# Optimization experiments

Measured on AMD Instinct MI355X. Metric: run time of the kernel, lower is better.

The kernel has to match this reference:

```python
import jax, jax.numpy as jnp
import numpy as np

D_MODEL = 1024
N_HEADS = 16
HEAD_DIM = D_MODEL // N_HEADS


def setup_inputs() -> dict:
    key = jax.random.key(0)
    k_x, k_wqkv, k_bqkv, k_wo, k_bo = jax.random.split(key, 5)
    b, t = 4, 2048
    s = 1.0 / np.sqrt(D_MODEL)
    return {
        "x": jax.random.normal(k_x, (b, t, D_MODEL), dtype=jnp.float32),
        "w_qkv": jax.random.uniform(k_wqkv, (D_MODEL, 3 * D_MODEL), jnp.float32, -s, s),
        "b_qkv": jax.random.uniform(k_bqkv, (3 * D_MODEL,), jnp.float32, -s, s),
        "w_out": jax.random.uniform(k_wo, (D_MODEL, D_MODEL), jnp.float32, -s, s),
        "b_out": jax.random.uniform(k_bo, (D_MODEL,), jnp.float32, -s, s),
    }


def reference(x, w_qkv, b_qkv, w_out, b_out):
    b, t, _ = x.shape
    # fused QKV projection -> [b, t, 3, h, d] -> q,k,v each [b, h, t, d]
    qkv = (x @ w_qkv + b_qkv).reshape(b, t, 3, N_HEADS, HEAD_DIM)
    q, k, v = jnp.moveaxis(qkv, 2, 0)          # each [b, t, h, d]
    q = q.transpose(0, 2, 1, 3)                # [b, h, t, d]
    k = k.transpose(0, 2, 1, 3)
    v = v.transpose(0, 2, 1, 3)
    scale = 1.0 / np.sqrt(HEAD_DIM).astype(np.float32)
    logits = jnp.einsum('bhqd,bhkd->bhqk', q, k) * scale
    causal = jnp.tril(jnp.ones((t, t), dtype=bool))
    logits = jnp.where(causal, logits, jnp.finfo(logits.dtype).min)
    attn = jax.nn.softmax(logits, axis=-1)
    out = jnp.einsum('bhqk,bhkd->bhqd', attn, v)      # [b, h, t, d]
    out = out.transpose(0, 2, 1, 3).reshape(b, t, D_MODEL)
    return out @ w_out + b_out
```

## Files before the change

kernel.cpp:

```cpp
#include <hip/hip_runtime.h>
#include <hip/hip_bf16.h>
#include <math.h>

#define NHEADS 16
#define HDIM   64
#define SEQT   2048
#define NBATCH 4
#define DMODEL 1024
#define MROWS  (NBATCH * SEQT)

typedef __bf16 bf16;
typedef bf16  bf16x8 __attribute__((ext_vector_type(8)));
typedef float f32x4  __attribute__((ext_vector_type(4)));
typedef float f32x16 __attribute__((ext_vector_type(16)));
typedef unsigned int u32x4 __attribute__((ext_vector_type(4)));

#define MFMA_BF16(a, b, c) __builtin_amdgcn_mfma_f32_16x16x32_bf16((a), (b), (c), 0, 0, 0)
#define MFMA32(a, b, c)    __builtin_amdgcn_mfma_f32_32x32x16_bf16((a), (b), (c), 0, 0, 0)
#define Z16 {0.f,0.f,0.f,0.f,0.f,0.f,0.f,0.f,0.f,0.f,0.f,0.f,0.f,0.f,0.f,0.f}
#define LOG2E 1.44269504f

__device__ __forceinline__ void gload_lds16(const void* g, void* l) {
  __builtin_amdgcn_global_load_lds((const __attribute__((address_space(1))) void*)g,
                                   (__attribute__((address_space(3))) void*)l, 16, 0, 0);
}

__device__ __forceinline__ unsigned cvtpk_bf16(float lo, float hi) {
  unsigned r;
  asm("v_cvt_pk_bf16_f32 %0, %1, %2" : "=v"(r) : "v"(lo), "v"(hi));
  return r;
}
__device__ __forceinline__ void plswap(unsigned& a, unsigned& b) {
  asm volatile("v_permlane32_swap_b32 %0, %1" : "+v"(a), "+v"(b));
}
__device__ __forceinline__ float exp2v(float x) {
  float r;
  asm("v_exp_f32 %0, %1" : "=v"(r) : "v"(x));
  return r;
}


__global__ __launch_bounds__(256) void k_cvt_f32_bf16(const float* __restrict__ in,
                                                      bf16* __restrict__ out, int n8) {
  int i = blockIdx.x * blockDim.x + threadIdx.x;
  if (i >= n8) return;
  const float4* in4 = (const float4*)in;
  float4 a = in4[(size_t)i * 2], b = in4[(size_t)i * 2 + 1];
  bf16x8 v;
  v[0] = (bf16)a.x; v[1] = (bf16)a.y; v[2] = (bf16)a.z; v[3] = (bf16)a.w;
  v[4] = (bf16)b.x; v[5] = (bf16)b.y; v[6] = (bf16)b.z; v[7] = (bf16)b.w;
  *(bf16x8*)(out + (size_t)i * 8) = v;
}

__global__ __launch_bounds__(256) void k_transpose_f32_bf16(const float* __restrict__ in,
                                                            bf16* __restrict__ out,
                                                            int R, int C) {
  int nct = C >> 6;
  int rt = blockIdx.x / nct, ct = blockIdx.x % nct;
  __shared__ float tile[64][65];
  int tid = threadIdx.x;
#pragma unroll
  for (int i = 0; i < 16; i++) {
    int e = i * 256 + tid, r = e >> 6, c = e & 63;
    tile[r][c] = in[(size_t)(rt * 64 + r) * C + ct * 64 + c];
  }
  __syncthreads();
#pragma unroll
  for (int i = 0; i < 16; i++) {
    int e = i * 256 + tid, r = e >> 6, c = e & 63;
    out[(size_t)(ct * 64 + r) * R + rt * 64 + c] = (bf16)tile[c][r];
  }
}

__global__ __launch_bounds__(256) void k_transpose_v(const bf16* __restrict__ v,
                                                     bf16* __restrict__ vt) {
  int tt = blockIdx.x & 31;
  int bh = blockIdx.x >> 5;
  __shared__ bf16 tile[64][65];
  int tid = threadIdx.x;
  const bf16* src = v + (size_t)bh * SEQT * 64 + (size_t)tt * 64 * 64;
#pragma unroll
  for (int i = 0; i < 16; i++) {
    int e = i * 256 + tid, r = e >> 6, c = e & 63;
    tile[r][c] = src[r * 64 + c];
  }
  __syncthreads();
  bf16* dst = vt + (size_t)bh * 64 * SEQT + tt * 64;
#pragma unroll
  for (int i = 0; i < 16; i++) {
    int e = i * 256 + tid, r = e >> 6, c = e & 63;
    dst[(size_t)r * SEQT + c] = tile[c][r];
  }
}


__device__ __forceinline__ void gemm128_core(const bf16* __restrict__ A,
                                             const bf16* __restrict__ Bt,
                                             int K, int bm, int bn, char* smem,
                                             f32x4 (&acc)[4][4]) {
  int tid = threadIdx.x, lane = tid & 63, w = tid >> 6;
  int l15 = lane & 15, g = lane >> 4;
  int wrow = (w >> 1) * 64, wcol = (w & 1) * 64;
  char* As = smem;
  char* Bs = smem + 8192;
  const char* Ag = (const char*)(A + (size_t)bm * 128 * K);
  const char* Bg = (const char*)(Bt + (size_t)bn * 128 * K);
  const int rowB = K * 2;
  int srow = w * 16 + (lane >> 2);
  int scol = (lane & 3) * 16;

  for (int kt = 0; kt < K / 32; kt++) {
#pragma unroll
    for (int is = 0; is < 2; is++) {
      int row = is * 64 + srow;
      gload_lds16(Ag + (size_t)row * rowB + kt * 64 + scol, As + is * 4096 + w * 1024);
      gload_lds16(Bg + (size_t)row * rowB + kt * 64 + scol, Bs + is * 4096 + w * 1024);
    }
    __syncthreads();
    bf16x8 af[4], bfr[4];
#pragma unroll
    for (int i = 0; i < 4; i++)
      af[i] = *(const bf16x8*)&As[(wrow + i * 16 + l15) * 64 + g * 16];
#pragma unroll
    for (int j = 0; j < 4; j++)
      bfr[j] = *(const bf16x8*)&Bs[(wcol + j * 16 + l15) * 64 + g * 16];
    __builtin_amdgcn_s_setprio(1);
#pragma unroll
    for (int i = 0; i < 4; i++)
#pragma unroll
      for (int j = 0; j < 4; j++)
        acc[i][j] = MFMA_BF16(af[i], bfr[j], acc[i][j]);
    __builtin_amdgcn_s_setprio(0);
    __syncthreads();
  }
}

__global__ __launch_bounds__(256) void k_gemm_qkv(const bf16* __restrict__ A,
                                                  const bf16* __restrict__ Bt,
                                                  const float* __restrict__ bias,
                                                  bf16* __restrict__ Qo,
                                                  bf16* __restrict__ Ko,
                                                  bf16* __restrict__ Vo) {
  const int K = DMODEL, NB = 24;
  int bid = (blockIdx.x & 7) * 192 + (blockIdx.x >> 3);
  int bm = bid / NB, bn = bid % NB;
  __shared__ __align__(16) char smem[16384];
  f32x4 acc[4][4] = {};
  gemm128_core(A, Bt, K, bm, bn, smem, acc);

  int tid = threadIdx.x, lane = tid & 63, w = tid >> 6;
  int l15 = lane & 15, g = lane >> 4;
  int wrow = (w >> 1) * 64, wcol = (w & 1) * 64;
  int rowbase = bm * 128 + wrow;
  int b = (bm * 128) >> 11;
#pragma unroll
  for (int j = 0; j < 4; j++) {
    int n = bn * 128 + wcol + j * 16 + l15;
    float bj = bias[n];
    int which = n >> 10;
    int nn = n & 1023;
    int head = nn >> 6, d = nn & 63;
    bf16* dst = (which == 0) ? Qo : (which == 1) ? Ko : Vo;
    size_t base = ((size_t)(b * NHEADS + head) * SEQT) * 64 + d;
#pragma unroll
    for (int i = 0; i < 4; i++) {
#pragma unroll
      for (int r = 0; r < 4; r++) {
        int row = rowbase + i * 16 + g * 4 + r;
        int t = row & (SEQT - 1);
        dst[base + (size_t)t * 64] = (bf16)(acc[i][j][r] + bj);
      }
    }
  }
}

__global__ __launch_bounds__(256) void k_gemm_out(const bf16* __restrict__ A,
                                                  const bf16* __restrict__ Bt,
                                                  const float* __restrict__ bias,
                                                  float* __restrict__ C) {
  const int K = DMODEL, NB = 8;
  int bid = (blockIdx.x & 7) * 64 + (blockIdx.x >> 3);
  int bm = bid / NB, bn = bid % NB;
  __shared__ __align__(16) char smem[16384];
  f32x4 acc[4][4] = {};
  gemm128_core(A, Bt, K, bm, bn, smem, acc);

  int tid = threadIdx.x, lane = tid & 63, w = tid >> 6;
  int l15 = lane & 15, g = lane >> 4;
  int wrow = (w >> 1) * 64, wcol = (w & 1) * 64;
#pragma unroll
  for (int j = 0; j < 4; j++) {
    int n = bn * 128 + wcol + j * 16 + l15;
    float bj = bias[n];
#pragma unroll
    for (int i = 0; i < 4; i++) {
#pragma unroll
      for (int r = 0; r < 4; r++) {
        int row = bm * 128 + wrow + i * 16 + g * 4 + r;
        C[(size_t)row * DMODEL + n] = acc[i][j][r] + bj;
      }
    }
  }
}


__global__ __launch_bounds__(128) void k_attn(const bf16* __restrict__ Q,
                                              const bf16* __restrict__ Kg,
                                              const bf16* __restrict__ VT,
                                              bf16* __restrict__ Oo) {
  int bh = blockIdx.x & 63;
  int qi = 31 - (blockIdx.x >> 6);
  int tid = threadIdx.x, lane = tid & 63, wv = tid >> 6;
  int l31 = lane & 31, hi = lane >> 5;
  __shared__ __align__(16) char smem[32768];

  const bf16* Qbh = Q + (size_t)bh * SEQT * 64;
  const char* Kbyte = (const char*)(Kg + (size_t)bh * SEQT * 64);
  const char* Vbyte = (const char*)(VT + (size_t)bh * 64 * SEQT);
  int qbase = qi * 64 + wv * 32;
  int ql = qbase + l31;

  int pp[4], lgK[4]; size_t vOff[4];
#pragma unroll
  for (int c = 0; c < 4; c++) {
    int p = c * 2048 + tid * 16;
    int row = p >> 7;
    int lg = p ^ ((row & 7) << 4);
    pp[c] = p; lgK[c] = lg;
    vOff[c] = (size_t)row * (SEQT * 2) + (lg & 127);
  }

  bf16x8 qf[4];
#pragma unroll
  for (int s = 0; s < 4; s++) {
    bf16x8 v = *(const bf16x8*)(Qbh + (size_t)ql * 64 + s * 16 + hi * 8);
#pragma unroll
    for (int e = 0; e < 8; e++) v[e] = (bf16)((float)v[e] * 0.125f);
    qf[s] = v;
  }

  bf16x8 onesf;
#pragma unroll
  for (int e = 0; e < 8; e++) onesf[e] = (bf16)1.0f;

  float m = -INFINITY;
  f32x16 o0 = Z16, o1 = Z16, lacc = Z16;

#pragma unroll
  for (int c = 0; c < 4; c++) {
    gload_lds16(Kbyte + lgK[c], smem + pp[c]);
    gload_lds16(Vbyte + vOff[c], smem + 16384 + pp[c]);
  }

  int NT = qi + 1;
  for (int t = 0; t < NT; t++) {
    __syncthreads();
    if (t + 1 < NT) {
      int nx = (t + 1) & 1;
      const char* kg = Kbyte + (size_t)(t + 1) * 8192;
      const char* vg = Vbyte + (size_t)(t + 1) * 128;
#pragma unroll
      for (int c = 0; c < 4; c++) {
        gload_lds16(kg + lgK[c], smem + nx * 8192 + pp[c]);
        gload_lds16(vg + vOff[c], smem + 16384 + nx * 8192 + pp[c]);
      }
    }
    const char* Ks = smem + (t & 1) * 8192;
    const char* Vs = smem + 16384 + (t & 1) * 8192;

    f32x16 st[2];
    __builtin_amdgcn_s_setprio(1);
#pragma unroll
    for (int h = 0; h < 2; h++) {
      f32x16 acc = Z16;
#pragma unroll
      for (int s = 0; s < 4; s++) {
        int row = h * 32 + l31;
        bf16x8 kf = *(const bf16x8*)&Ks[(row * 128 + s * 32 + hi * 16) ^ ((l31 & 7) << 4)];
        acc = MFMA32(kf, qf[s], acc);
      }
      st[h] = acc;
    }
    __builtin_amdgcn_s_setprio(0);

    if (t == NT - 1) {
      int rel = ql - (t * 64 + 4 * hi);
#pragma unroll
      for (int r = 0; r < 16; r++) {
        const int R0 = (r & 3) + 8 * (r >> 2);
        if (R0 > rel) st[0][r] = -INFINITY;
        if (R0 > rel - 32) st[1][r] = -INFINITY;
      }
    }

    float m0 = -INFINITY, m1 = -INFINITY, m2 = -INFINITY, m3 = -INFINITY;
#pragma unroll
    for (int h = 0; h < 2; h++)
#pragma unroll
      for (int r = 0; r < 16; r += 4) {
        m0 = fmaxf(m0, st[h][r]);
        m1 = fmaxf(m1, st[h][r + 1]);
        m2 = fmaxf(m2, st[h][r + 2]);
        m3 = fmaxf(m3, st[h][r + 3]);
      }
    float mx = fmaxf(fmaxf(m0, m1), fmaxf(m2, m3));
    mx = fmaxf(mx, __shfl_xor(mx, 32));

    if (__any(mx > m + 8.f)) {
      float mn = fmaxf(m, mx);
      float co = exp2v((m - mn) * LOG2E);
      m = mn;
#pragma unroll
      for (int r = 0; r < 16; r++) {
        const int R0 = (r & 3) + 8 * (r >> 2);
        float fac = __shfl(co, R0 + 4 * hi);
        o0[r] *= fac; o1[r] *= fac; lacc[r] *= fac;
      }
    }

    float negmq = -m * LOG2E;
#pragma unroll
    for (int h = 0; h < 2; h++)
#pragma unroll
      for (int r = 0; r < 16; r++)
        st[h][r] = exp2v(fmaf(st[h][r], LOG2E, negmq));

    __builtin_amdgcn_s_setprio(1);
#pragma unroll
    for (int h = 0; h < 2; h++) {
      unsigned pw[8];
#pragma unroll
      for (int i = 0; i < 8; i++) pw[i] = cvtpk_bf16(st[h][2 * i], st[h][2 * i + 1]);
      plswap(pw[0], pw[2]); plswap(pw[1], pw[3]);
      plswap(pw[4], pw[6]); plswap(pw[5], pw[7]);
      u32x4 f0 = {pw[0], pw[1], pw[2], pw[3]};
      u32x4 f1 = {pw[4], pw[5], pw[6], pw[7]};
      bf16x8 pa0 = __builtin_bit_cast(bf16x8, f0);
      bf16x8 pa1 = __builtin_bit_cast(bf16x8, f1);
      lacc = MFMA32(pa0, onesf, lacc);
      lacc = MFMA32(pa1, onesf, lacc);
      {
        int vrow = l31;
        bf16x8 bv0 = *(const bf16x8*)&Vs[(vrow * 128 + (2 * h) * 32 + hi * 16) ^ ((l31 & 7) << 4)];
        bf16x8 bv1 = *(const bf16x8*)&Vs[(vrow * 128 + (2 * h + 1) * 32 + hi * 16) ^ ((l31 & 7) << 4)];
        o0 = MFMA32(pa0, bv0, o0);
        o0 = MFMA32(pa1, bv1, o0);
      }
      {
        int vrow = 32 + l31;
        bf16x8 bv0 = *(const bf16x8*)&Vs[(vrow * 128 + (2 * h) * 32 + hi * 16) ^ ((l31 & 7) << 4)];
        bf16x8 bv1 = *(const bf16x8*)&Vs[(vrow * 128 + (2 * h + 1) * 32 + hi * 16) ^ ((l31 & 7) << 4)];
        o1 = MFMA32(pa0, bv0, o1);
        o1 = MFMA32(pa1, bv1, o1);
      }
    }
    __builtin_amdgcn_s_setprio(0);
  }

  int b = bh >> 4, hd = bh & 15;
#pragma unroll
  for (int r = 0; r < 16; r++) {
    const int R0 = (r & 3) + 8 * (r >> 2);
    int qrow = qbase + R0 + 4 * hi;
    float inv = 1.f / lacc[r];
    size_t off = ((size_t)(b * SEQT + qrow)) * DMODEL + hd * 64;
    Oo[off + l31]      = (bf16)(o0[r] * inv);
    Oo[off + 32 + l31] = (bf16)(o1[r] * inv);
  }
}


extern "C" void kernel_launch(void* const* d_in, const int* in_sizes, int n_in,
                              void* d_out, int out_size, void* d_ws, size_t ws_size,
                              hipStream_t stream) {
  const float* x     = (const float*)d_in[0];
  const float* w_qkv = (const float*)d_in[1];
  const float* b_qkv = (const float*)d_in[2];
  const float* w_out = (const float*)d_in[3];
  const float* b_out = (const float*)d_in[4];
  float* out = (float*)d_out;

  char* ws = (char*)d_ws;
  bf16* xb    = (bf16*)(ws);
  bf16* wqkvT = (bf16*)(ws + (16u << 20));
  bf16* woutT = (bf16*)(ws + (22u << 20));
  bf16* Qb    = (bf16*)(ws + (24u << 20));
  bf16* Kb    = (bf16*)(ws + (40u << 20));
  bf16* Vb    = (bf16*)(ws + (56u << 20));
  bf16* VTb   = (bf16*)(ws + (72u << 20));
  bf16* attn_o = xb;

  k_cvt_f32_bf16<<<(MROWS * DMODEL / 8 + 255) / 256, 256, 0, stream>>>(x, xb, MROWS * DMODEL / 8);
  k_transpose_f32_bf16<<<16 * 48, 256, 0, stream>>>(w_qkv, wqkvT, DMODEL, 3 * DMODEL);
  k_transpose_f32_bf16<<<16 * 16, 256, 0, stream>>>(w_out, woutT, DMODEL, DMODEL);
  k_gemm_qkv<<<64 * 24, 256, 0, stream>>>(xb, wqkvT, b_qkv, Qb, Kb, Vb);
  k_transpose_v<<<64 * 32, 256, 0, stream>>>(Vb, VTb);
  k_attn<<<32 * 64, 128, 0, stream>>>(Qb, Kb, VTb, attn_o);
  k_gemm_out<<<64 * 8, 256, 0, stream>>>(attn_o, woutT, b_out, out);
}
```

Before: 268.7 us.

## Load V directly into registers, halve attention LDS, drop GEMM swizzle and setprio

In the attention kernel, V tiles are no longer staged through shared memory. Each lane now reads its V fragments straight from global memory into registers every iteration, which halves the LDS footprint, and the launch bounds ask for 3 blocks per CU to raise occupancy. Separately, the GEMM kernels drop the blockIdx remapping that grouped tiles for cache locality, and the shared GEMM core drops its s_setprio around the MFMA loop. The V loads now sit on the critical path with no prefetch, and removing the block remap can reduce L2 reuse.

```diff
diff --git a/kernel.cpp b/kernel.cpp
--- a/kernel.cpp
+++ b/kernel.cpp
@@ -124,13 +124,11 @@
 #pragma unroll
     for (int j = 0; j < 4; j++)
       bfr[j] = *(const bf16x8*)&Bs[(wcol + j * 16 + l15) * 64 + g * 16];
-    __builtin_amdgcn_s_setprio(1);
 #pragma unroll
     for (int i = 0; i < 4; i++)
 #pragma unroll
       for (int j = 0; j < 4; j++)
         acc[i][j] = MFMA_BF16(af[i], bfr[j], acc[i][j]);
-    __builtin_amdgcn_s_setprio(0);
     __syncthreads();
   }
 }
@@ -142,8 +140,7 @@
                                                   bf16* __restrict__ Ko,
                                                   bf16* __restrict__ Vo) {
   const int K = DMODEL, NB = 24;
-  int bid = (blockIdx.x & 7) * 192 + (blockIdx.x >> 3);
-  int bm = bid / NB, bn = bid % NB;
+  int bm = blockIdx.x / NB, bn = blockIdx.x % NB;
   __shared__ __align__(16) char smem[16384];
   f32x4 acc[4][4] = {};
   gemm128_core(A, Bt, K, bm, bn, smem, acc);
@@ -179,8 +176,7 @@
                                                   const float* __restrict__ bias,
                                                   float* __restrict__ C) {
   const int K = DMODEL, NB = 8;
-  int bid = (blockIdx.x & 7) * 64 + (blockIdx.x >> 3);
-  int bm = bid / NB, bn = bid % NB;
+  int bm = blockIdx.x / NB, bn = blockIdx.x % NB;
   __shared__ __align__(16) char smem[16384];
   f32x4 acc[4][4] = {};
   gemm128_core(A, Bt, K, bm, bn, smem, acc);
@@ -204,15 +200,15 @@
 }
 
 
-__global__ __launch_bounds__(128) void k_attn(const bf16* __restrict__ Q,
-                                              const bf16* __restrict__ Kg,
-                                              const bf16* __restrict__ VT,
-                                              bf16* __restrict__ Oo) {
+__global__ __launch_bounds__(128, 3) void k_attn(const bf16* __restrict__ Q,
+                                                 const bf16* __restrict__ Kg,
+                                                 const bf16* __restrict__ VT,
+                                                 bf16* __restrict__ Oo) {
   int bh = blockIdx.x & 63;
   int qi = 31 - (blockIdx.x >> 6);
   int tid = threadIdx.x, lane = tid & 63, wv = tid >> 6;
   int l31 = lane & 31, hi = lane >> 5;
-  __shared__ __align__(16) char smem[32768];
+  __shared__ __align__(16) char smem[16384];
 
   const bf16* Qbh = Q + (size_t)bh * SEQT * 64;
   const char* Kbyte = (const char*)(Kg + (size_t)bh * SEQT * 64);
@@ -220,15 +216,16 @@
   int qbase = qi * 64 + wv * 32;
   int ql = qbase + l31;
 
-  int pp[4], lgK[4]; size_t vOff[4];
+  int pp[4], lgK[4];
 #pragma unroll
   for (int c = 0; c < 4; c++) {
     int p = c * 2048 + tid * 16;
     int row = p >> 7;
-    int lg = p ^ ((row & 7) << 4);
-    pp[c] = p; lgK[c] = lg;
-    vOff[c] = (size_t)row * (SEQT * 2) + (lg & 127);
-  }
+    pp[c] = p; lgK[c] = p ^ ((row & 7) << 4);
+  }
+
+  const char* vb0 = Vbyte + (size_t)l31 * (SEQT * 2) + hi * 16;
+  const char* vb1 = Vbyte + (size_t)(32 + l31) * (SEQT * 2) + hi * 16;
 
   bf16x8 qf[4];
 #pragma unroll
@@ -247,10 +244,8 @@
   f32x16 o0 = Z16, o1 = Z16, lacc = Z16;
 
 #pragma unroll
-  for (int c = 0; c < 4; c++) {
+  for (int c = 0; c < 4; c++)
     gload_lds16(Kbyte + lgK[c], smem + pp[c]);
-    gload_lds16(Vbyte + vOff[c], smem + 16384 + pp[c]);
-  }
 
   int NT = qi + 1;
   for (int t = 0; t < NT; t++) {
@@ -258,15 +253,20 @@
     if (t + 1 < NT) {
       int nx = (t + 1) & 1;
       const char* kg = Kbyte + (size_t)(t + 1) * 8192;
-      const char* vg = Vbyte + (size_t)(t + 1) * 128;
-#pragma unroll
-      for (int c = 0; c < 4; c++) {
+#pragma unroll
+      for (int c = 0; c < 4; c++)
         gload_lds16(kg + lgK[c], smem + nx * 8192 + pp[c]);
-        gload_lds16(vg + vOff[c], smem + 16384 + nx * 8192 + pp[c]);
-      }
     }
     const char* Ks = smem + (t & 1) * 8192;
-    const char* Vs = smem + 16384 + (t & 1) * 8192;
+
+    const char* v0t = vb0 + (size_t)t * 128;
+    const char* v1t = vb1 + (size_t)t * 128;
+    bf16x8 bv0[4], bv1[4];
+#pragma unroll
+    for (int ks = 0; ks < 4; ks++) {
+      bv0[ks] = *(const bf16x8*)(v0t + ks * 32);
+      bv1[ks] = *(const bf16x8*)(v1t + ks * 32);
+    }
 
     f32x16 st[2];
     __builtin_amdgcn_s_setprio(1);
@@ -339,20 +339,10 @@
       bf16x8 pa1 = __builtin_bit_cast(bf16x8, f1);
       lacc = MFMA32(pa0, onesf, lacc);
       lacc = MFMA32(pa1, onesf, lacc);
-      {
-        int vrow = l31;
-        bf16x8 bv0 = *(const bf16x8*)&Vs[(vrow * 128 + (2 * h) * 32 + hi * 16) ^ ((l31 & 7) << 4)];
-        bf16x8 bv1 = *(const bf16x8*)&Vs[(vrow * 128 + (2 * h + 1) * 32 + hi * 16) ^ ((l31 & 7) << 4)];
-        o0 = MFMA32(pa0, bv0, o0);
-        o0 = MFMA32(pa1, bv1, o0);
-      }
-      {
-        int vrow = 32 + l31;
-        bf16x8 bv0 = *(const bf16x8*)&Vs[(vrow * 128 + (2 * h) * 32 + hi * 16) ^ ((l31 & 7) << 4)];
-        bf16x8 bv1 = *(const bf16x8*)&Vs[(vrow * 128 + (2 * h + 1) * 32 + hi * 16) ^ ((l31 & 7) << 4)];
-        o1 = MFMA32(pa0, bv0, o1);
-        o1 = MFMA32(pa1, bv1, o1);
-      }
+      o0 = MFMA32(pa0, bv0[2 * h], o0);
+      o0 = MFMA32(pa1, bv0[2 * h + 1], o0);
+      o1 = MFMA32(pa0, bv1[2 * h], o1);
+      o1 = MFMA32(pa1, bv1[2 * h + 1], o1);
     }
     __builtin_amdgcn_s_setprio(0);
   }
```

Measured after the change: 284.6 us. 1.06x slower.
